# Kernel optimization log

Measured on AMD Instinct MI355X. Metric: run time of the kernel, lower is better.

Reference implementation:

```python
import jax, jax.numpy as jnp
import numpy as np

BLOCK = 64      # InformationEntropyAnalyzer block_size
BINS = 256      # InformationEntropyAnalyzer num_bins
EPS = 1e-12


def setup_inputs() -> dict:
    key = jax.random.key(0)
    x = jax.random.normal(key, (8, 64, 256, 256), dtype=jnp.float32)
    return {"x": x}


def _block_entropy(blocks):
    """Shannon entropy per block, matching np.histogram(density=True) math.

    blocks: (B, n) float32. Returns (B,) float32.
    """
    B, n = blocks.shape
    bmin = jnp.min(blocks, axis=1, keepdims=True)            # (B,1)
    bmax = jnp.max(blocks, axis=1, keepdims=True)            # (B,1)
    width = (bmax - bmin) / BINS                              # uniform bin width
    width_safe = jnp.where(width > 0, width, 1.0)
    # np.histogram: rightmost edge inclusive -> floor + clip reproduces it
    idx = jnp.clip(jnp.floor((blocks - bmin) / width_safe), 0, BINS - 1).astype(jnp.int32)
    row = jnp.arange(B, dtype=jnp.int32)[:, None]
    flat = (row * BINS + idx).reshape(-1)
    counts = jax.ops.segment_sum(
        jnp.ones((B * n,), jnp.float32), flat, num_segments=B * BINS
    ).reshape(B, BINS)
    density = counts / (n * width_safe)                       # density=True normalization
    p = density + EPS
    p = p / jnp.sum(p, axis=1, keepdims=True)
    return -jnp.sum(p * jnp.log2(p), axis=1)


def reference(x):
    """Faithful JAX version of InformationEntropyAnalyzer._compute_4d_entropy.

    Per (n,c) slice: split HxW into BLOCKxBLOCK tiles, compute Shannon entropy
    of the 256-bin histogram of each tile, then bilinearly upsample
    (align_corners=False, i.e. half-pixel, = jax.image.resize 'linear')
    back to (H, W).  Output: (N, C, H, W) entropy map.
    """
    N, C, H, W = x.shape
    nbh, nbw = H // BLOCK, W // BLOCK  # evenly divisible by construction
    blocks = (
        x.reshape(N, C, nbh, BLOCK, nbw, BLOCK)
        .transpose(0, 1, 2, 4, 3, 5)
        .reshape(N * C * nbh * nbw, BLOCK * BLOCK)
    )
    ent = _block_entropy(blocks).reshape(N, C, nbh, nbw)
    # F.interpolate(mode='bilinear', align_corners=False) == half-pixel linear resize
    return jax.image.resize(ent, (N, C, H, W), method='linear')
```

## Files before the change

### kernel.cpp

```cpp
#include <hip/hip_runtime.h>

#define NBINS 256
#define EPSF 1e-12f

typedef float v4f __attribute__((ext_vector_type(4)));

__global__ __launch_bounds__(256, 2) void fused_kernel(const float* __restrict__ x,
                                                       float* __restrict__ out) {
    const int nc   = blockIdx.x;
    const int t    = threadIdx.x;
    const int lane = t & 63;
    const int wave = t >> 6;

    __shared__ unsigned int hist[4][NBINS];
    __shared__ float ent_s[16];

    const float* cbase = x + ((size_t)nc << 16) + (size_t)wave * 64;
    unsigned int* h = hist[wave];

    v4f va[16], vb[16];

#define ISSUE(buf, s)                                                             \
    _Pragma("unroll")                                                             \
    for (int k = 0; k < 16; ++k) {                                                \
        const int f = lane + (k << 6);                    \
        buf[k] = *reinterpret_cast<const v4f*>(                                   \
            cbase + (size_t)(s) * (64 * 256) + (size_t)(f >> 4) * 256 + (f & 15) * 4); \
    }

#define PROCESS(buf, s)                                                           \
    {                                                                             \
        float lmin = INFINITY, lmax = -INFINITY;                                  \
        _Pragma("unroll")                                                         \
        for (int k = 0; k < 16; ++k) {                                            \
            lmin = fminf(lmin, fminf(fminf(buf[k].x, buf[k].y),                   \
                                     fminf(buf[k].z, buf[k].w)));                 \
            lmax = fmaxf(lmax, fmaxf(fmaxf(buf[k].x, buf[k].y),                   \
                                     fmaxf(buf[k].z, buf[k].w)));                 \
        }                                                                         \
        _Pragma("unroll")                                                         \
        for (int off = 32; off > 0; off >>= 1) {                                  \
            lmin = fminf(lmin, __shfl_xor(lmin, off));                            \
            lmax = fmaxf(lmax, __shfl_xor(lmax, off));                            \
        }                                                                         \
        uint4 z; z.x = z.y = z.z = z.w = 0u;       \
        reinterpret_cast<uint4*>(h)[lane] = z;                                    \
        const float width = (lmax - lmin) * (1.0f / NBINS);                       \
        const float wsafe = (width > 0.0f) ? width : 1.0f;                        \
        const float inv   = 1.0f / wsafe;                                         \
        const float coff  = -lmin * inv;                                          \
        _Pragma("unroll")                                                         \
        for (int k = 0; k < 16; ++k) {                                            \
            float vals[4] = {buf[k].x, buf[k].y, buf[k].z, buf[k].w};             \
            _Pragma("unroll")                                                     \
            for (int j = 0; j < 4; ++j) {                                         \
                      \
                int bin = (int)fmaf(vals[j], inv, coff);                          \
                bin = min(bin, 255);                                              \
                atomicAdd(&h[bin], 1u);                                           \
            }                                                                     \
        }                                                                         \
        const uint4 c    = reinterpret_cast<const uint4*>(h)[lane];               \
        const float pden = inv * (1.0f / 4096.0f);            \
        const float p0 = (float)c.x * pden + EPSF;                                \
        const float p1 = (float)c.y * pden + EPSF;                                \
        const float p2 = (float)c.z * pden + EPSF;                                \
        const float p3 = (float)c.w * pden + EPSF;                                \
        float s_ = p0 + p1 + p2 + p3;                                             \
        _Pragma("unroll")                                                         \
        for (int off = 32; off > 0; off >>= 1) s_ += __shfl_xor(s_, off);         \
        const float itot = 1.0f / s_;                                             \
        const float q0 = p0 * itot, q1 = p1 * itot;                               \
        const float q2 = p2 * itot, q3 = p3 * itot;                               \
        float e = q0 * log2f(q0) + q1 * log2f(q1)                                 \
                + q2 * log2f(q2) + q3 * log2f(q3);                                \
        _Pragma("unroll")                                                         \
        for (int off = 32; off > 0; off >>= 1) e += __shfl_xor(e, off);           \
        if (lane == 0) ent_s[((s) << 2) + wave] = -e;                             \
    }

    const int x4 = lane;
    const int ix = (int)floorf(((x4 << 2) + 0.5f) * 0.015625f - 0.5f);
    const int x0 = max(ix, 0), x1 = min(ix + 1, 3);
    v4f wv[4];
#pragma unroll
    for (int j = 0; j < 4; ++j) {
        const float fx = ((x4 << 2) + j + 0.5f) * 0.015625f - 0.5f;
        const float wx = fx - floorf(fx);
        const float a  = 1.0f - wx, bb = wx;
        wv[j].x = ((x0 == 0) ? a : 0.0f) + ((x1 == 0) ? bb : 0.0f);
        wv[j].y = ((x0 == 1) ? a : 0.0f) + ((x1 == 1) ? bb : 0.0f);
        wv[j].z = ((x0 == 2) ? a : 0.0f) + ((x1 == 2) ? bb : 0.0f);
        wv[j].w = ((x0 == 3) ? a : 0.0f) + ((x1 == 3) ? bb : 0.0f);
    }
    const v4f* er = reinterpret_cast<const v4f*>(ent_s);
    v4f* out4 = reinterpret_cast<v4f*>(out) + ((size_t)nc << 14);

#define WR(ystart, nrows)                                                         \
    _Pragma("unroll")                                                             \
    for (int i = 0; i < (nrows) / 4; ++i) {                                       \
        const int   y   = (ystart) + wave * ((nrows) / 4) + i;                    \
        const float fy  = (y + 0.5f) * 0.015625f - 0.5f;                          \
        const float fiy = floorf(fy);                                             \
        const float wy  = fy - fiy;                                               \
        const int   iy  = (int)fiy;                                               \
        const int   y0  = max(iy, 0), y1 = min(iy + 1, 3);                        \
        const v4f r0 = er[y0];                 \
        const v4f r1 = er[y1];                                                    \
        v4f rv = r0 * (1.0f - wy) + r1 * wy;                                      \
        v4f o;                                                                    \
        o.x = rv.x * wv[0].x + rv.y * wv[0].y + rv.z * wv[0].z + rv.w * wv[0].w;  \
        o.y = rv.x * wv[1].x + rv.y * wv[1].y + rv.z * wv[1].z + rv.w * wv[1].w;  \
        o.z = rv.x * wv[2].x + rv.y * wv[2].y + rv.z * wv[2].z + rv.w * wv[2].w;  \
        o.w = rv.x * wv[3].x + rv.y * wv[3].y + rv.z * wv[3].z + rv.w * wv[3].w;  \
        out4[(y << 6) + lane] = o;                                                \
    }

    ISSUE(va, 0)
    ISSUE(vb, 1)
    PROCESS(va, 0)
    ISSUE(va, 2)
    __syncthreads();
    WR(0, 32)
    PROCESS(vb, 1)
    ISSUE(vb, 3)
    __syncthreads();
    WR(32, 64)
    PROCESS(va, 2)
    __syncthreads();
    WR(96, 64)
    PROCESS(vb, 3)
    __syncthreads();
    WR(160, 96)

#undef ISSUE
#undef PROCESS
#undef WR
}

extern "C" void kernel_launch(void* const* d_in, const int* in_sizes, int n_in,
                              void* d_out, int out_size, void* d_ws, size_t ws_size,
                              hipStream_t stream) {
    const float* x   = (const float*)d_in[0];
    float*       out = (float*)d_out;
    fused_kernel<<<512, 256, 0, stream>>>(x, out);
}
```

Baseline: 45.59 us.

## Double waves per block so each wave handles two tile-rows instead of four

Each block now runs 512 threads (8 waves) instead of 256. Waves 0-3 histogram tile-rows 0 and 1, and waves 4-7 histogram tile-rows 3 and 2, which halves each wave's serial chain of load, histogram and entropy work. The output is written in two phases. Rows 0-31 and 224-255 need only edge entropies, so they are written after the first sync. The middle 192 rows are split across the 8 waves after the second sync. This raises the number of waves resident per CU to hide memory latency, at the cost of more LDS histograms and the register pressure of launch_bounds(512,2) with two 16-vector load buffers.

```diff
diff --git a/kernel.cpp b/kernel.cpp
--- a/kernel.cpp
+++ b/kernel.cpp
@@ -5,17 +5,20 @@
 
 typedef float v4f __attribute__((ext_vector_type(4)));
 
-__global__ __launch_bounds__(256, 2) void fused_kernel(const float* __restrict__ x,
+__global__ __launch_bounds__(512, 2) void fused_kernel(const float* __restrict__ x,
                                                        float* __restrict__ out) {
     const int nc   = blockIdx.x;
     const int t    = threadIdx.x;
     const int lane = t & 63;
     const int wave = t >> 6;
+    const int col  = wave & 3;
+    const int rA   = (wave < 4) ? 0 : 3;
+    const int rB   = (wave < 4) ? 1 : 2;
 
-    __shared__ unsigned int hist[4][NBINS];
+    __shared__ unsigned int hist[8][NBINS];
     __shared__ float ent_s[16];
 
-    const float* cbase = x + ((size_t)nc << 16) + (size_t)wave * 64;
+    const float* cbase = x + ((size_t)nc << 16) + (size_t)col * 64;
     unsigned int* h = hist[wave];
 
     v4f va[16], vb[16];
@@ -76,7 +79,7 @@
                 + q2 * log2f(q2) + q3 * log2f(q3);                                \
         _Pragma("unroll")                                                         \
         for (int off = 32; off > 0; off >>= 1) e += __shfl_xor(e, off);           \
-        if (lane == 0) ent_s[((s) << 2) + wave] = -e;                             \
+        if (lane == 0) ent_s[((s) << 2) + col] = -e;                              \
     }
 
     const int x4 = lane;
@@ -98,8 +101,8 @@
 
 #define WR(ystart, nrows)                                                         \
     _Pragma("unroll")                                                             \
-    for (int i = 0; i < (nrows) / 4; ++i) {                                       \
-        const int   y   = (ystart) + wave * ((nrows) / 4) + i;                    \
+    for (int i = 0; i < (nrows); ++i) {                                           \
+        const int   y   = (ystart) + i;                                           \
         const float fy  = (y + 0.5f) * 0.015625f - 0.5f;                          \
         const float fiy = floorf(fy);                                             \
         const float wy  = fy - fiy;                                               \
@@ -116,22 +119,17 @@
         out4[(y << 6) + lane] = o;                                                \
     }
 
-    ISSUE(va, 0)
-    ISSUE(vb, 1)
-    PROCESS(va, 0)
-    ISSUE(va, 2)
+    ISSUE(va, rA)
+    ISSUE(vb, rB)
+    PROCESS(va, rA)
     __syncthreads();
-    WR(0, 32)
-    PROCESS(vb, 1)
-    ISSUE(vb, 3)
+    {
+        const int ystart = (wave < 4) ? (wave << 3) : (192 + (wave << 3));
+        WR(ystart, 8)
+    }
+    PROCESS(vb, rB)
     __syncthreads();
-    WR(32, 64)
-    PROCESS(va, 2)
-    __syncthreads();
-    WR(96, 64)
-    PROCESS(vb, 3)
-    __syncthreads();
-    WR(160, 96)
+    WR(32 + wave * 24, 24)
 
 #undef ISSUE
 #undef PROCESS
@@ -143,5 +141,5 @@
                               hipStream_t stream) {
     const float* x   = (const float*)d_in[0];
     float*       out = (float*)d_out;
-    fused_kernel<<<512, 256, 0, stream>>>(x, out);
+    fused_kernel<<<512, 512, 0, stream>>>(x, out);
 }
```

Result: slower. 51.63 us (+13.3%).
